# Kernel optimization log

Measured on AMD Instinct MI355X. Metric: run time of the kernel, lower is better.

The kernel has to match this reference:

```python
import jax, jax.numpy as jnp
import numpy as np

B, NOBJ = 64, 16
NUM_CLASSES = 91
IOU_TH = 0.5
NEG_POS = 3
VAR0, VAR1 = 0.1, 0.2
IMG = 300.0


def _ssd300_priors():
    # Standard SSD300 PriorBox: 8732 priors in center-size form (cx, cy, w, h), normalized to [0,1]
    fmaps = [38, 19, 10, 5, 3, 1]
    steps = [8, 16, 32, 64, 100, 300]
    min_s = [30, 60, 111, 162, 213, 264]
    max_s = [60, 111, 162, 213, 264, 315]
    ars = [[2], [2, 3], [2, 3], [2, 3], [2], [2]]
    out = []
    for k, f in enumerate(fmaps):
        for i in range(f):
            for j in range(f):
                cx = (j + 0.5) * steps[k] / IMG
                cy = (i + 0.5) * steps[k] / IMG
                s = min_s[k] / IMG
                out.append([cx, cy, s, s])
                sp = float(np.sqrt(s * max_s[k] / IMG))
                out.append([cx, cy, sp, sp])
                for ar in ars[k]:
                    r = float(np.sqrt(ar))
                    out.append([cx, cy, s * r, s / r])
                    out.append([cx, cy, s / r, s * r])
    return np.clip(np.asarray(out, np.float32), 0.0, 1.0)


def setup_inputs() -> dict:
    priors = jnp.asarray(_ssd300_priors())  # [8732, 4]
    P = priors.shape[0]
    key = jax.random.key(0)
    k1, k2, k3, k4, k5 = jax.random.split(key, 5)
    loc_data = jax.random.normal(k1, (B, P, 4), jnp.float32)
    conf_data = jax.random.normal(k2, (B, P, NUM_CLASSES), jnp.float32)
    centers = jax.random.uniform(k3, (B, NOBJ, 2), minval=40.0, maxval=260.0)
    half = jax.random.uniform(k5, (B, NOBJ, 2), minval=10.0, maxval=40.0)
    gt_boxes = jnp.concatenate([centers - half, centers + half], axis=-1)  # point form, pixel coords
    gt_labels = jax.random.randint(k4, (B, NOBJ), 1, NUM_CLASSES).astype(jnp.int32)
    return {"loc_data": loc_data, "conf_data": conf_data, "gt_boxes": gt_boxes,
            "gt_labels": gt_labels, "priors": priors}


def _point_form(pr):
    return jnp.concatenate([pr[:, :2] - pr[:, 2:] / 2, pr[:, :2] + pr[:, 2:] / 2], axis=1)


def _jaccard(boxes, pboxes):
    # boxes [N,4], pboxes [P,4] both point form -> IoU [N,P]
    lt = jnp.maximum(boxes[:, None, :2], pboxes[None, :, :2])
    rb = jnp.minimum(boxes[:, None, 2:], pboxes[None, :, 2:])
    wh = jnp.clip(rb - lt, 0.0)
    inter = wh[..., 0] * wh[..., 1]
    area_a = ((boxes[:, 2] - boxes[:, 0]) * (boxes[:, 3] - boxes[:, 1]))[:, None]
    area_b = ((pboxes[:, 2] - pboxes[:, 0]) * (pboxes[:, 3] - pboxes[:, 1]))[None, :]
    return inter / (area_a + area_b - inter)


def _encode(matched, priors):
    # matched [P,4] point form, priors [P,4] center-size form
    g_cxcy = ((matched[:, :2] + matched[:, 2:]) / 2 - priors[:, :2]) / (VAR0 * priors[:, 2:])
    g_wh = jnp.log((matched[:, 2:] - matched[:, :2]) / priors[:, 2:]) / VAR1
    return jnp.concatenate([g_cxcy, g_wh], axis=1)


def _match(boxes, labels, priors):
    # boxes [NOBJ,4] normalized point form; labels [NOBJ]; priors [P,4]
    ov = _jaccard(boxes, _point_form(priors))            # [NOBJ, P]
    best_prior_idx = jnp.argmax(ov, axis=1)              # [NOBJ]
    best_truth_ov = jnp.max(ov, axis=0)                  # [P]
    best_truth_idx = jnp.argmax(ov, axis=0)              # [P]
    best_truth_ov = best_truth_ov.at[best_prior_idx].set(2.0)
    for j in range(NOBJ):  # small fixed loop, matches torch in-order scatter
        best_truth_idx = best_truth_idx.at[best_prior_idx[j]].set(j)
    matched = boxes[best_truth_idx]                      # [P,4]
    conf = labels[best_truth_idx]
    conf = jnp.where(best_truth_ov < IOU_TH, 0, conf)
    return _encode(matched, priors), conf


def reference(loc_data, conf_data, gt_boxes, gt_labels, priors):
    P = priors.shape[0]
    loc_t, conf_t = jax.vmap(lambda b, l: _match(b / IMG, l, priors))(gt_boxes, gt_labels)
    pos = conf_t > 0                                      # [B,P]
    # localization loss: SmoothL1 (beta=1), summed over positives
    diff = loc_data - loc_t
    ad = jnp.abs(diff)
    sl1 = jnp.where(ad < 1.0, 0.5 * diff * diff, ad - 0.5)
    loss_l = jnp.sum(sl1 * pos[..., None].astype(sl1.dtype))
    # hard negative mining on per-prior CE loss
    lse = jax.nn.logsumexp(conf_data, axis=-1)            # [B,P]
    gathered = jnp.take_along_axis(conf_data, conf_t[..., None].astype(jnp.int32), axis=-1)[..., 0]
    ce_all = lse - gathered                                # [B,P]
    mine = jnp.where(pos, 0.0, ce_all)
    order = jnp.argsort(-mine, axis=1)
    rank = jnp.argsort(order, axis=1)
    num_pos = jnp.sum(pos, axis=1, keepdims=True)
    num_neg = jnp.clip(NEG_POS * num_pos, 1, P - 1)
    neg = rank < num_neg
    mask = pos | neg
    loss_c = jnp.sum(ce_all * mask.astype(ce_all.dtype))
    N = jnp.maximum(jnp.sum(num_pos).astype(jnp.float32), 1.0)
    return jnp.stack([loss_l / N, loss_c / N])  # [loss_l, loss_c]
```

## Files before the change

### kernel.cpp

```cpp
#include <hip/hip_runtime.h>
#include <math.h>

#define BATCH 64
#define NOBJ 16
#define NPRIOR 8732
#define NC 91
#define IMG 300.0f
#define GPB 1092
#define NGROUP (GPB * BATCH)
#define CE_GRID 6144
#define GBINS 2048
#define HB 16
#define HCHUNK 546
#define MSPLIT 16
#define SL 546

__global__ __launch_bounds__(256) void k_match1(
    const float* __restrict__ loc_data,
    const float* __restrict__ gt_boxes,
    const int*   __restrict__ gt_labels,
    const float* __restrict__ priors,
    int*   __restrict__ conf_t,
    float* __restrict__ ll_part,
    int*   __restrict__ np_part,
    float* __restrict__ candv,
    int*   __restrict__ candi)
{
    __shared__ float bx0[NOBJ], by0[NOBJ], bx1[NOBJ], by1[NOBJ], barea[NOBJ];
    __shared__ int   blab[NOBJ];
    __shared__ float rv[NOBJ][4];
    __shared__ int   ri[NOBJ][4];
    __shared__ float red_f[4];
    __shared__ int   red_i[4];

    const int b    = blockIdx.y;
    const int blk  = blockIdx.x;
    const int tid  = threadIdx.x;
    const int lane = tid & 63;
    const int wave = tid >> 6;
    const int p0   = blk * SL;
    const int pend = min(p0 + SL, NPRIOR);

    if (tid < NOBJ) {
        float4 g = ((const float4*)gt_boxes)[(size_t)b * NOBJ + tid];
        float x0 = g.x * (1.0f / IMG), y0 = g.y * (1.0f / IMG);
        float x1 = g.z * (1.0f / IMG), y1 = g.w * (1.0f / IMG);
        bx0[tid] = x0; by0[tid] = y0; bx1[tid] = x1; by1[tid] = y1;
        barea[tid] = (x1 - x0) * (y1 - y0);
        blab[tid] = gt_labels[b * NOBJ + tid];
    }
    __syncthreads();

    float bv[NOBJ];
    int   bi[NOBJ];
#pragma unroll
    for (int j = 0; j < NOBJ; j++) { bv[j] = -1.0f; bi[j] = 0x7fffffff; }

    int np_local = 0;
    float ll_local = 0.0f;

    for (int p = p0 + tid; p < pend; p += 256) {
        float4 pr = ((const float4*)priors)[p];
        float cx = pr.x, cy = pr.y, w = pr.z, h = pr.w;
        float px0 = cx - 0.5f * w, py0 = cy - 0.5f * h;
        float px1 = cx + 0.5f * w, py1 = cy + 0.5f * h;
        float pa = w * h;
        float maxv = -1.0f; int maxj = 0;
        float mx0 = 0, my0 = 0, mx1 = 0, my1 = 0;
#pragma unroll
        for (int j = 0; j < NOBJ; j++) {
            float ltx = fmaxf(bx0[j], px0), lty = fmaxf(by0[j], py0);
            float rbx = fminf(bx1[j], px1), rby = fminf(by1[j], py1);
            float iw = fmaxf(rbx - ltx, 0.0f), ih = fmaxf(rby - lty, 0.0f);
            float inter = iw * ih;
            float iou = inter / (barea[j] + pa - inter);
            if (iou > maxv) {
                maxv = iou; maxj = j;
                mx0 = bx0[j]; my0 = by0[j]; mx1 = bx1[j]; my1 = by1[j];
            }
            if (iou > bv[j]) { bv[j] = iou; bi[j] = p; }
        }
        int conf = (maxv < 0.5f) ? 0 : blab[maxj];
        conf_t[(size_t)b * NPRIOR + p] = conf;
        if (conf > 0) {
            np_local++;
            float g0 = ((mx0 + mx1) * 0.5f - cx) / (0.1f * w);
            float g1 = ((my0 + my1) * 0.5f - cy) / (0.1f * h);
            float g2 = logf((mx1 - mx0) / w) * 5.0f;
            float g3 = logf((my1 - my0) / h) * 5.0f;
            float4 lv = ((const float4*)loc_data)[(size_t)b * NPRIOR + p];
            float d0 = lv.x - g0, d1 = lv.y - g1, d2 = lv.z - g2, d3 = lv.w - g3;
            float a0 = fabsf(d0), a1 = fabsf(d1), a2 = fabsf(d2), a3 = fabsf(d3);
            ll_local += (a0 < 1.f ? 0.5f * d0 * d0 : a0 - 0.5f)
                      + (a1 < 1.f ? 0.5f * d1 * d1 : a1 - 0.5f)
                      + (a2 < 1.f ? 0.5f * d2 * d2 : a2 - 0.5f)
                      + (a3 < 1.f ? 0.5f * d3 * d3 : a3 - 0.5f);
        }
    }

#pragma unroll
    for (int j = 0; j < NOBJ; j++) {
        float v = bv[j]; int ix = bi[j];
        for (int off = 32; off; off >>= 1) {
            float v2 = __shfl_xor(v, off);
            int   i2 = __shfl_xor(ix, off);
            if (v2 > v || (v2 == v && i2 < ix)) { v = v2; ix = i2; }
        }
        if (lane == 0) { rv[j][wave] = v; ri[j][wave] = ix; }
    }
    for (int off = 32; off; off >>= 1) {
        ll_local += __shfl_xor(ll_local, off);
        np_local += __shfl_xor(np_local, off);
    }
    if (lane == 0) { red_f[wave] = ll_local; red_i[wave] = np_local; }
    __syncthreads();
    if (tid < NOBJ) {
        int j = tid;
        float v = rv[j][0]; int ix = ri[j][0];
#pragma unroll
        for (int w2 = 1; w2 < 4; w2++) {
            float v2 = rv[j][w2]; int i2 = ri[j][w2];
            if (v2 > v || (v2 == v && i2 < ix)) { v = v2; ix = i2; }
        }
        size_t o = ((size_t)b * MSPLIT + blk) * NOBJ + j;
        candv[o] = v;
        candi[o] = ix;
    }
    if (tid == 0) {
        ll_part[b * MSPLIT + blk] = red_f[0] + red_f[1] + red_f[2] + red_f[3];
        np_part[b * MSPLIT + blk] = red_i[0] + red_i[1] + red_i[2] + red_i[3];
    }
}

__global__ __launch_bounds__(64) void k_bpi(
    const float* __restrict__ candv,
    const int*   __restrict__ candi,
    int* __restrict__ bpi_g)
{
    const int b = blockIdx.x;
    const int j = threadIdx.x;
    if (j < NOBJ) {
        size_t base = (size_t)b * MSPLIT * NOBJ + j;
        float v = candv[base]; int ix = candi[base];
#pragma unroll
        for (int c = 1; c < MSPLIT; c++) {
            float v2 = candv[base + c * NOBJ];
            int   i2 = candi[base + c * NOBJ];
            if (v2 > v || (v2 == v && i2 < ix)) { v = v2; ix = i2; }
        }
        bpi_g[b * NOBJ + j] = ix;
    }
}

__global__ __launch_bounds__(64) void k_fix(
    const float* __restrict__ loc_data,
    const float* __restrict__ gt_boxes,
    const int*   __restrict__ gt_labels,
    const float* __restrict__ priors,
    const int*   __restrict__ bpi_g,
    int*   __restrict__ conf_t,
    float* __restrict__ ll_fix,
    int*   __restrict__ np_fix)
{
    const int b = blockIdx.x;
    const int lane = threadIdx.x;

    float ll_d = 0.0f;
    int   np_d = 0;

    if (lane < NOBJ) {
        const int j = lane;
        const int ps = bpi_g[b * NOBJ + j];
        bool last = true;
        for (int j2 = j + 1; j2 < NOBJ; j2++)
            if (bpi_g[b * NOBJ + j2] == ps) last = false;
        if (last) {
            float4 pr = ((const float4*)priors)[ps];
            float cx = pr.x, cy = pr.y, w = pr.z, h = pr.w;
            float px0 = cx - 0.5f * w, py0 = cy - 0.5f * h;
            float px1 = cx + 0.5f * w, py1 = cy + 0.5f * h;
            float pa = w * h;
            float maxv = -1.0f;
            float mx0 = 0, my0 = 0, mx1 = 0, my1 = 0;
            float jx0 = 0, jy0 = 0, jx1 = 0, jy1 = 0;
            for (int j2 = 0; j2 < NOBJ; j2++) {
                float4 g = ((const float4*)gt_boxes)[(size_t)b * NOBJ + j2];
                float x0 = g.x * (1.0f / IMG), y0 = g.y * (1.0f / IMG);
                float x1 = g.z * (1.0f / IMG), y1 = g.w * (1.0f / IMG);
                float area = (x1 - x0) * (y1 - y0);
                float ltx = fmaxf(x0, px0), lty = fmaxf(y0, py0);
                float rbx = fminf(x1, px1), rby = fminf(y1, py1);
                float iw = fmaxf(rbx - ltx, 0.0f), ih = fmaxf(rby - lty, 0.0f);
                float inter = iw * ih;
                float iou = inter / (area + pa - inter);
                if (iou > maxv) { maxv = iou; mx0 = x0; my0 = y0; mx1 = x1; my1 = y1; }
                if (j2 == j)    { jx0 = x0; jy0 = y0; jx1 = x1; jy1 = y1; }
            }
            float4 lv = ((const float4*)loc_data)[(size_t)b * NPRIOR + ps];
            if (maxv >= 0.5f) {
                float g0 = ((mx0 + mx1) * 0.5f - cx) / (0.1f * w);
                float g1 = ((my0 + my1) * 0.5f - cy) / (0.1f * h);
                float g2 = logf((mx1 - mx0) / w) * 5.0f;
                float g3 = logf((my1 - my0) / h) * 5.0f;
                float d0 = lv.x - g0, d1 = lv.y - g1, d2 = lv.z - g2, d3 = lv.w - g3;
                float a0 = fabsf(d0), a1 = fabsf(d1), a2 = fabsf(d2), a3 = fabsf(d3);
                ll_d -= (a0 < 1.f ? 0.5f * d0 * d0 : a0 - 0.5f)
                      + (a1 < 1.f ? 0.5f * d1 * d1 : a1 - 0.5f)
                      + (a2 < 1.f ? 0.5f * d2 * d2 : a2 - 0.5f)
                      + (a3 < 1.f ? 0.5f * d3 * d3 : a3 - 0.5f);
                np_d -= 1;
            }
            {
                float g0 = ((jx0 + jx1) * 0.5f - cx) / (0.1f * w);
                float g1 = ((jy0 + jy1) * 0.5f - cy) / (0.1f * h);
                float g2 = logf((jx1 - jx0) / w) * 5.0f;
                float g3 = logf((jy1 - jy0) / h) * 5.0f;
                float d0 = lv.x - g0, d1 = lv.y - g1, d2 = lv.z - g2, d3 = lv.w - g3;
                float a0 = fabsf(d0), a1 = fabsf(d1), a2 = fabsf(d2), a3 = fabsf(d3);
                ll_d += (a0 < 1.f ? 0.5f * d0 * d0 : a0 - 0.5f)
                      + (a1 < 1.f ? 0.5f * d1 * d1 : a1 - 0.5f)
                      + (a2 < 1.f ? 0.5f * d2 * d2 : a2 - 0.5f)
                      + (a3 < 1.f ? 0.5f * d3 * d3 : a3 - 0.5f);
                np_d += 1;
            }
            conf_t[(size_t)b * NPRIOR + ps] = gt_labels[b * NOBJ + j];
        }
    }

    for (int off = 32; off; off >>= 1) {
        ll_d += __shfl_xor(ll_d, off);
        np_d += __shfl_xor(np_d, off);
    }
    if (lane == 0) { ll_fix[b] = ll_d; np_fix[b] = np_d; }
}

#define CE_ISSUE(gg, R0, R1, R2, NF)                                           \
    {   int b_ = (gg) / GPB, ci_ = (gg) - b_ * GPB;                            \
        int p0_ = ci_ * 8;                                                     \
        int rows_ = min(8, NPRIOR - p0_);                                      \
        NF = (rows_ * NC) >> 2;                                                \
        const float4* s_ = (const float4*)(conf_data + ((size_t)b_ * NPRIOR + p0_) * NC); \
        R0 = s_[tid];                                                          \
        if (tid + 64  < NF) R1 = s_[tid + 64];                                 \
        if (tid + 128 < NF) R2 = s_[tid + 128]; }

#define CT_LOAD(gg)                                                            \
    ( conf_t[(size_t)((gg) / GPB) * NPRIOR + ((gg) - ((gg) / GPB) * GPB) * 8 + (tid >> 3)] )

#define CE_WRITE(BUF, R0, R1, R2, NF)                                          \
    {   float4* d_ = (float4*)sbuf[BUF];                                       \
        d_[tid] = R0;                                                          \
        if (tid + 64  < NF) d_[tid + 64]  = R1;                                \
        if (tid + 128 < NF) d_[tid + 128] = R2; }

#define CE_COMPUTE(gg, BUF, TG)                                                \
    {   int b_ = (gg) / GPB, ci_ = (gg) - b_ * GPB;                            \
        int p0_ = ci_ * 8;                                                     \
        int rows_ = min(8, NPRIOR - p0_);                                      \
        int rr_ = tid >> 3, q_ = tid & 7;                                      \
        if (rr_ < rows_) {                                                     \
            const float* row_ = sbuf[BUF] + rr_ * NC;                          \
            float s_ = 0.0f;                                                   \
            _Pragma("unroll")                                                  \
            for (int i_ = q_; i_ < NC; i_ += 8) s_ += __expf(row_[i_]);        \
            s_ += __shfl_xor(s_, 1);                                           \
            s_ += __shfl_xor(s_, 2);                                           \
            s_ += __shfl_xor(s_, 4);                                           \
            if (q_ == 0) {                                                     \
                size_t o_ = (size_t)b_ * NPRIOR + p0_ + rr_;                   \
                int tgt_ = TG;                                                 \
                float ce_ = __logf(s_) - row_[tgt_];                           \
                if (tgt_ > 0) { pos_acc += ce_; mine[o_] = 0.0f; }             \
                else          { mine[o_] = fmaxf(ce_, 0.0f); }                 \
            } } }

__global__ __launch_bounds__(64) void k_ce(
    const float* __restrict__ conf_data,
    const int*   __restrict__ conf_t,
    float* __restrict__ mine,
    float* __restrict__ lc_part)
{
    __shared__ float sbuf[2][8 * NC];
    const int tid = threadIdx.x;
    const int G = CE_GRID;

    float4 a0, a1, a2, b0, b1, b2;
    int nfA = 0, nfB = 0;
    float pos_acc = 0.0f;

    int g = blockIdx.x;
    CE_ISSUE(g, a0, a1, a2, nfA);
    int tcur = CT_LOAD(g);
    if (g + G < NGROUP) CE_ISSUE(g + G, b0, b1, b2, nfB);
    CE_WRITE(0, a0, a1, a2, nfA);

    for (; g < NGROUP; g += 2 * G) {
        int tnext = (g + G < NGROUP) ? CT_LOAD(g + G) : 0;
        if (g + 2 * G < NGROUP) CE_ISSUE(g + 2 * G, a0, a1, a2, nfA);
        CE_COMPUTE(g, 0, tcur);
        if (g + G < NGROUP) {
            CE_WRITE(1, b0, b1, b2, nfB);
            int tn2 = (g + 2 * G < NGROUP) ? CT_LOAD(g + 2 * G) : 0;
            if (g + 3 * G < NGROUP) CE_ISSUE(g + 3 * G, b0, b1, b2, nfB);
            CE_COMPUTE(g + G, 1, tnext);
            if (g + 2 * G < NGROUP) CE_WRITE(0, a0, a1, a2, nfA);
            tcur = tn2;
        }
    }

    for (int off = 32; off; off >>= 1) pos_acc += __shfl_xor(pos_acc, off);
    if (tid == 0) lc_part[blockIdx.x] = pos_acc;
}

__global__ __launch_bounds__(256) void k_hist(
    const float* __restrict__ mine,
    int*   __restrict__ ghc,
    float* __restrict__ gsc)
{
    __shared__ int   lh[GBINS];
    __shared__ float ls[GBINS];

    const int b  = blockIdx.y;
    const int ci = blockIdx.x;
    const int tid = threadIdx.x;
    const int i0 = ci * HCHUNK;
    const int iend = min(i0 + HCHUNK, NPRIOR);

#pragma unroll
    for (int j = 0; j < GBINS / 256; j++) {
        lh[tid + j * 256] = 0;
        ls[tid + j * 256] = 0.0f;
    }
    __syncthreads();

    for (int i = i0 + tid; i < iend; i += 256) {
        float v = mine[(size_t)b * NPRIOR + i];
        int bin = min((int)(v * 128.0f), GBINS - 1);
        atomicAdd(&lh[bin], 1);
        atomicAdd(&ls[bin], v);
    }
    __syncthreads();

    const size_t base = ((size_t)b * HB + ci) * GBINS;
#pragma unroll
    for (int j = 0; j < GBINS / 256; j++) {
        int bin = tid + j * 256;
        ghc[base + bin] = lh[bin];
        gsc[base + bin] = ls[bin];
    }
}

__global__ __launch_bounds__(1024) void k_sel(
    const int*   __restrict__ ghc,
    const float* __restrict__ gsc,
    const int*   __restrict__ np_part,
    const int*   __restrict__ np_fix,
    float* __restrict__ lc2)
{
    __shared__ int   wtot[16];
    __shared__ int   s_B0, s_r;
    __shared__ float red_f[16];

    const int b = blockIdx.x;
    const int tid = threadIdx.x;
    const int lane = tid & 63;
    const int wave = tid >> 6;

    int   c0 = 0, c1 = 0;
    float m0 = 0.0f, m1 = 0.0f;
    const size_t base = (size_t)b * HB * GBINS;
#pragma unroll
    for (int c = 0; c < HB; c++) {
        c0 += ghc[base + (size_t)c * GBINS + 2 * tid];
        c1 += ghc[base + (size_t)c * GBINS + 2 * tid + 1];
        m0 += gsc[base + (size_t)c * GBINS + 2 * tid];
        m1 += gsc[base + (size_t)c * GBINS + 2 * tid + 1];
    }

    int np = np_fix[b];
#pragma unroll
    for (int c = 0; c < MSPLIT; c++) np += np_part[b * MSPLIT + c];
    const int kk = min(max(3 * np, 1), NPRIOR - 1);

    const int ps = c0 + c1;
    int incl = ps;
#pragma unroll
    for (int off = 1; off < 64; off <<= 1) {
        int t = __shfl_down(incl, off);
        incl += (lane + off < 64) ? t : 0;
    }
    if (lane == 0) wtot[wave] = incl;
    __syncthreads();
    int hi = 0;
#pragma unroll
    for (int w = 0; w < 16; w++) if (w > wave) hi += wtot[w];
    const int suf = (incl - ps) + hi;
    if (suf < kk && kk <= suf + c1)          { s_B0 = 2 * tid + 1; s_r = kk - suf; }
    const int suf1 = suf + c1;
    if (suf1 < kk && kk <= suf1 + c0)        { s_B0 = 2 * tid;     s_r = kk - suf1; }
    __syncthreads();

    const int B0 = s_B0;
    const int r  = s_r;

    float sg = 0.0f;
    if (2 * tid     > B0) sg += m0;
    if (2 * tid + 1 > B0) sg += m1;
    if      (2 * tid     == B0) sg += (float)r * (m0 / (float)c0);
    else if (2 * tid + 1 == B0) sg += (float)r * (m1 / (float)c1);

    for (int off = 32; off; off >>= 1) sg += __shfl_xor(sg, off);
    if (lane == 0) red_f[wave] = sg;
    __syncthreads();
    if (tid == 0) {
        float s = 0.0f;
#pragma unroll
        for (int w = 0; w < 16; w++) s += red_f[w];
        lc2[b] = s;
    }
}

__global__ __launch_bounds__(1024) void k_final(
    const float* __restrict__ lc_part, const float* __restrict__ lc2,
    const float* __restrict__ ll_part, const int* __restrict__ np_part,
    const float* __restrict__ ll_fix, const int* __restrict__ np_fix,
    float* __restrict__ out)
{
    __shared__ float rf[16][2];
    __shared__ int   rn[16];
    const int tid = threadIdx.x;
    float lc = 0.0f;
    for (int i = tid; i < CE_GRID; i += 1024) lc += lc_part[i];
    float ll = 0.0f; int np = 0;
    if (tid < BATCH) { lc += lc2[tid]; ll += ll_fix[tid]; np += np_fix[tid]; }
    if (tid < BATCH * MSPLIT) { ll += ll_part[tid]; np += np_part[tid]; }
    for (int off = 32; off; off >>= 1) {
        lc += __shfl_xor(lc, off);
        ll += __shfl_xor(ll, off);
        np += __shfl_xor(np, off);
    }
    const int lane = tid & 63, wave = tid >> 6;
    if (lane == 0) { rf[wave][0] = lc; rf[wave][1] = ll; rn[wave] = np; }
    __syncthreads();
    if (tid == 0) {
        float lcT = 0.0f, llT = 0.0f; int npT = 0;
        for (int w = 0; w < 16; w++) { lcT += rf[w][0]; llT += rf[w][1]; npT += rn[w]; }
        float N = fmaxf((float)npT, 1.0f);
        out[0] = llT / N;
        out[1] = lcT / N;
    }
}

extern "C" void kernel_launch(void* const* d_in, const int* in_sizes, int n_in,
                              void* d_out, int out_size, void* d_ws, size_t ws_size,
                              hipStream_t stream)
{
    const float* loc_data  = (const float*)d_in[0];
    const float* conf_data = (const float*)d_in[1];
    const float* gt_boxes  = (const float*)d_in[2];
    const int*   gt_labels = (const int*)d_in[3];
    const float* priors    = (const float*)d_in[4];
    float* out = (float*)d_out;

    char* ws = (char*)d_ws;
    float* ll_part  = (float*)(ws + 0);
    int*   np_part  = (int*)(ws + 4096);
    float* lc2      = (float*)(ws + 8192);
    float* ll_fix   = (float*)(ws + 8704);
    int*   np_fix   = (int*)(ws + 9216);
    float* lc_part  = (float*)(ws + 12288);
    int*   conf_t   = (int*)(ws + 65536);
    float* mine     = (float*)(ws + 65536 + 2235392);
    float* candv    = (float*)(ws + 7340032);
    int*   candi    = (int*)(ws + 7405568);
    int*   bpi_g    = (int*)(ws + 7471104);
    int*   ghc      = (int*)(ws + 16777216);
    float* gsc      = (float*)(ws + 25165824);

    hipLaunchKernelGGL(k_match1, dim3(MSPLIT, BATCH), dim3(256), 0, stream,
                       loc_data, gt_boxes, gt_labels, priors,
                       conf_t, ll_part, np_part, candv, candi);
    hipLaunchKernelGGL(k_bpi, dim3(BATCH), dim3(64), 0, stream,
                       candv, candi, bpi_g);
    hipLaunchKernelGGL(k_fix, dim3(BATCH), dim3(64), 0, stream,
                       loc_data, gt_boxes, gt_labels, priors, bpi_g,
                       conf_t, ll_fix, np_fix);
    hipLaunchKernelGGL(k_ce, dim3(CE_GRID), dim3(64), 0, stream,
                       conf_data, conf_t, mine, lc_part);
    hipLaunchKernelGGL(k_hist, dim3(HB, BATCH), dim3(256), 0, stream,
                       mine, ghc, gsc);
    hipLaunchKernelGGL(k_sel, dim3(BATCH), dim3(1024), 0, stream,
                       ghc, gsc, np_part, np_fix, lc2);
    hipLaunchKernelGGL(k_final, dim3(1), dim3(1024), 0, stream,
                       lc_part, lc2, ll_part, np_part, ll_fix, np_fix, out);
}
```

Before: 104.7 us.

## Fuse best-prior reduction into fix kernel and histogram into selection kernel

Merges the per-object best-prior reduction with the forced-match fixup kernel, passing indices through shared memory instead of global memory. Merges the per-chunk histogram kernel with the threshold-selection kernel, so each batch builds its full 2048-bin histogram in shared memory and selects the top-k cutoff in place. This removes two kernel launches and the large global partial-histogram write and read. In exchange, histogram building runs on only one block per batch image, which reduces parallelism.

```diff
diff --git a/kernel.cpp b/kernel.cpp
--- a/kernel.cpp
+++ b/kernel.cpp
@@ -10,8 +10,6 @@
 #define NGROUP (GPB * BATCH)
 #define CE_GRID 6144
 #define GBINS 2048
-#define HB 16
-#define HCHUNK 546
 #define MSPLIT 16
 #define SL 546
 
@@ -132,15 +130,23 @@
     }
 }
 
-__global__ __launch_bounds__(64) void k_bpi(
+__global__ __launch_bounds__(64) void k_bpi_fix(
+    const float* __restrict__ loc_data,
+    const float* __restrict__ gt_boxes,
+    const int*   __restrict__ gt_labels,
+    const float* __restrict__ priors,
     const float* __restrict__ candv,
     const int*   __restrict__ candi,
-    int* __restrict__ bpi_g)
-{
+    int*   __restrict__ conf_t,
+    float* __restrict__ ll_fix,
+    int*   __restrict__ np_fix)
+{
+    __shared__ int bpi_s[NOBJ];
     const int b = blockIdx.x;
-    const int j = threadIdx.x;
-    if (j < NOBJ) {
-        size_t base = (size_t)b * MSPLIT * NOBJ + j;
+    const int lane = threadIdx.x;
+
+    if (lane < NOBJ) {
+        size_t base = (size_t)b * MSPLIT * NOBJ + lane;
         float v = candv[base]; int ix = candi[base];
 #pragma unroll
         for (int c = 1; c < MSPLIT; c++) {
@@ -148,32 +154,19 @@
             int   i2 = candi[base + c * NOBJ];
             if (v2 > v || (v2 == v && i2 < ix)) { v = v2; ix = i2; }
         }
-        bpi_g[b * NOBJ + j] = ix;
-    }
-}
-
-__global__ __launch_bounds__(64) void k_fix(
-    const float* __restrict__ loc_data,
-    const float* __restrict__ gt_boxes,
-    const int*   __restrict__ gt_labels,
-    const float* __restrict__ priors,
-    const int*   __restrict__ bpi_g,
-    int*   __restrict__ conf_t,
-    float* __restrict__ ll_fix,
-    int*   __restrict__ np_fix)
-{
-    const int b = blockIdx.x;
-    const int lane = threadIdx.x;
+        bpi_s[lane] = ix;
+    }
+    __syncthreads();
 
     float ll_d = 0.0f;
     int   np_d = 0;
 
     if (lane < NOBJ) {
         const int j = lane;
-        const int ps = bpi_g[b * NOBJ + j];
+        const int ps = bpi_s[j];
         bool last = true;
         for (int j2 = j + 1; j2 < NOBJ; j2++)
-            if (bpi_g[b * NOBJ + j2] == ps) last = false;
+            if (bpi_s[j2] == ps) last = false;
         if (last) {
             float4 pr = ((const float4*)priors)[ps];
             float cx = pr.x, cy = pr.y, w = pr.z, h = pr.w;
@@ -312,19 +305,22 @@
     if (tid == 0) lc_part[blockIdx.x] = pos_acc;
 }
 
-__global__ __launch_bounds__(256) void k_hist(
+__global__ __launch_bounds__(256) void k_histsel(
     const float* __restrict__ mine,
-    int*   __restrict__ ghc,
-    float* __restrict__ gsc)
+    const int*   __restrict__ np_part,
+    const int*   __restrict__ np_fix,
+    float* __restrict__ lc2)
 {
     __shared__ int   lh[GBINS];
     __shared__ float ls[GBINS];
-
-    const int b  = blockIdx.y;
-    const int ci = blockIdx.x;
+    __shared__ int   wtot[4];
+    __shared__ int   s_B0, s_r;
+    __shared__ float red_f[4];
+
+    const int b = blockIdx.x;
     const int tid = threadIdx.x;
-    const int i0 = ci * HCHUNK;
-    const int iend = min(i0 + HCHUNK, NPRIOR);
+    const int lane = tid & 63;
+    const int wave = tid >> 6;
 
 #pragma unroll
     for (int j = 0; j < GBINS / 256; j++) {
@@ -333,57 +329,28 @@
     }
     __syncthreads();
 
-    for (int i = i0 + tid; i < iend; i += 256) {
+    for (int i = tid; i < NPRIOR; i += 256) {
         float v = mine[(size_t)b * NPRIOR + i];
         int bin = min((int)(v * 128.0f), GBINS - 1);
         atomicAdd(&lh[bin], 1);
         atomicAdd(&ls[bin], v);
     }
-    __syncthreads();
-
-    const size_t base = ((size_t)b * HB + ci) * GBINS;
-#pragma unroll
-    for (int j = 0; j < GBINS / 256; j++) {
-        int bin = tid + j * 256;
-        ghc[base + bin] = lh[bin];
-        gsc[base + bin] = ls[bin];
-    }
-}
-
-__global__ __launch_bounds__(1024) void k_sel(
-    const int*   __restrict__ ghc,
-    const float* __restrict__ gsc,
-    const int*   __restrict__ np_part,
-    const int*   __restrict__ np_fix,
-    float* __restrict__ lc2)
-{
-    __shared__ int   wtot[16];
-    __shared__ int   s_B0, s_r;
-    __shared__ float red_f[16];
-
-    const int b = blockIdx.x;
-    const int tid = threadIdx.x;
-    const int lane = tid & 63;
-    const int wave = tid >> 6;
-
-    int   c0 = 0, c1 = 0;
-    float m0 = 0.0f, m1 = 0.0f;
-    const size_t base = (size_t)b * HB * GBINS;
-#pragma unroll
-    for (int c = 0; c < HB; c++) {
-        c0 += ghc[base + (size_t)c * GBINS + 2 * tid];
-        c1 += ghc[base + (size_t)c * GBINS + 2 * tid + 1];
-        m0 += gsc[base + (size_t)c * GBINS + 2 * tid];
-        m1 += gsc[base + (size_t)c * GBINS + 2 * tid + 1];
-    }
 
     int np = np_fix[b];
 #pragma unroll
     for (int c = 0; c < MSPLIT; c++) np += np_part[b * MSPLIT + c];
     const int kk = min(max(3 * np, 1), NPRIOR - 1);
-
-    const int ps = c0 + c1;
-    int incl = ps;
+    __syncthreads();
+
+    int   cnt[8];
+    float sm[8];
+#pragma unroll
+    for (int j = 0; j < 8; j++) { cnt[j] = lh[tid * 8 + j]; sm[j] = ls[tid * 8 + j]; }
+    int own = 0;
+#pragma unroll
+    for (int j = 0; j < 8; j++) own += cnt[j];
+
+    int incl = own;
 #pragma unroll
     for (int off = 1; off < 64; off <<= 1) {
         int t = __shfl_down(incl, off);
@@ -393,31 +360,33 @@
     __syncthreads();
     int hi = 0;
 #pragma unroll
-    for (int w = 0; w < 16; w++) if (w > wave) hi += wtot[w];
-    const int suf = (incl - ps) + hi;
-    if (suf < kk && kk <= suf + c1)          { s_B0 = 2 * tid + 1; s_r = kk - suf; }
-    const int suf1 = suf + c1;
-    if (suf1 < kk && kk <= suf1 + c0)        { s_B0 = 2 * tid;     s_r = kk - suf1; }
-    __syncthreads();
-
+    for (int w = 0; w < 4; w++) if (w > wave) hi += wtot[w];
+    const int suf = (incl - own) + hi;
+
+    int found = -1;
+    int s2 = suf;
+#pragma unroll
+    for (int j = 7; j >= 0; j--) {
+        if (found < 0 && s2 < kk && kk <= s2 + cnt[j])
+            found = (tid * 8 + j) * 16384 + (kk - s2);
+        s2 += cnt[j];
+    }
+    if (found >= 0) { s_B0 = found >> 14; s_r = found & 16383; }
+    __syncthreads();
     const int B0 = s_B0;
     const int r  = s_r;
 
     float sg = 0.0f;
-    if (2 * tid     > B0) sg += m0;
-    if (2 * tid + 1 > B0) sg += m1;
-    if      (2 * tid     == B0) sg += (float)r * (m0 / (float)c0);
-    else if (2 * tid + 1 == B0) sg += (float)r * (m1 / (float)c1);
-
+#pragma unroll
+    for (int j = 0; j < 8; j++) {
+        int bin = tid * 8 + j;
+        if (bin > B0)       sg += sm[j];
+        else if (bin == B0) sg += (float)r * (sm[j] / (float)cnt[j]);
+    }
     for (int off = 32; off; off >>= 1) sg += __shfl_xor(sg, off);
     if (lane == 0) red_f[wave] = sg;
     __syncthreads();
-    if (tid == 0) {
-        float s = 0.0f;
-#pragma unroll
-        for (int w = 0; w < 16; w++) s += red_f[w];
-        lc2[b] = s;
-    }
+    if (tid == 0) lc2[b] = red_f[0] + red_f[1] + red_f[2] + red_f[3];
 }
 
 __global__ __launch_bounds__(1024) void k_final(
@@ -473,24 +442,17 @@
     float* mine     = (float*)(ws + 65536 + 2235392);
     float* candv    = (float*)(ws + 7340032);
     int*   candi    = (int*)(ws + 7405568);
-    int*   bpi_g    = (int*)(ws + 7471104);
-    int*   ghc      = (int*)(ws + 16777216);
-    float* gsc      = (float*)(ws + 25165824);
 
     hipLaunchKernelGGL(k_match1, dim3(MSPLIT, BATCH), dim3(256), 0, stream,
                        loc_data, gt_boxes, gt_labels, priors,
                        conf_t, ll_part, np_part, candv, candi);
-    hipLaunchKernelGGL(k_bpi, dim3(BATCH), dim3(64), 0, stream,
-                       candv, candi, bpi_g);
-    hipLaunchKernelGGL(k_fix, dim3(BATCH), dim3(64), 0, stream,
-                       loc_data, gt_boxes, gt_labels, priors, bpi_g,
+    hipLaunchKernelGGL(k_bpi_fix, dim3(BATCH), dim3(64), 0, stream,
+                       loc_data, gt_boxes, gt_labels, priors, candv, candi,
                        conf_t, ll_fix, np_fix);
     hipLaunchKernelGGL(k_ce, dim3(CE_GRID), dim3(64), 0, stream,
                        conf_data, conf_t, mine, lc_part);
-    hipLaunchKernelGGL(k_hist, dim3(HB, BATCH), dim3(256), 0, stream,
-                       mine, ghc, gsc);
-    hipLaunchKernelGGL(k_sel, dim3(BATCH), dim3(1024), 0, stream,
-                       ghc, gsc, np_part, np_fix, lc2);
+    hipLaunchKernelGGL(k_histsel, dim3(BATCH), dim3(256), 0, stream,
+                       mine, np_part, np_fix, lc2);
     hipLaunchKernelGGL(k_final, dim3(1), dim3(1024), 0, stream,
                        lc_part, lc2, ll_part, np_part, ll_fix, np_fix, out);
 }
```

Result: no change. 103.5 us (-1.1%).
